# Performance work log

Measured on AMD Instinct MI355X. Metric: run time of the kernel, lower is better.

Reference implementation:

```python
import jax, jax.numpy as jnp
import numpy as np

R = 65  # num_relations


def rgcn_conv(x, edge_index, edge_type, W, root, bias):
    """PyG RGCNConv with per-relation mean aggregation.
    Aggregate-then-transform (linearity lets us swap the order):
      mean_r[n] = mean over edges e with type r, dst(e)=n of x[src(e)]
      out = sum_r mean_r @ W_r + x @ root + bias
    """
    N = x.shape[0]
    src, dst = edge_index[0], edge_index[1]
    seg = edge_type * N + dst  # composite (relation, dst) segment id
    sums = jax.ops.segment_sum(x[src], seg, num_segments=R * N)
    sums = sums.reshape(R, N, -1)  # [R, N, F]
    cnt = jax.ops.segment_sum(jnp.ones(src.shape, x.dtype), seg, num_segments=R * N)
    cnt = cnt.reshape(R, N, 1)
    mean = sums / jnp.maximum(cnt, 1.0)
    return jnp.einsum('rni,rio->no', mean, W) + x @ root + bias


def setup_inputs() -> dict:
    key = jax.random.key(0)
    ks = jax.random.split(key, 20)
    N, E, F_in, H, M = 8000, 192000, 64, 256, 64
    B = 128
    inp = {
        'x': jax.random.normal(ks[0], (N, F_in), jnp.float32),
        'edge_index': jax.random.randint(ks[1], (2, E), 0, N),
        'edge_type': jax.random.randint(ks[2], (E,), 0, R),
        'batch': jnp.sort(jax.random.randint(ks[3], (N,), 0, B)),
    }
    def glorot(k, shape):
        fan = shape[-2] + shape[-1]
        return jax.random.normal(k, shape, jnp.float32) * jnp.sqrt(2.0 / fan)
    inp['W1'] = glorot(ks[4], (R, F_in, H)); inp['root1'] = glorot(ks[5], (F_in, H)); inp['b1'] = jnp.zeros((H,), jnp.float32)
    inp['W2'] = glorot(ks[6], (R, H, H));   inp['root2'] = glorot(ks[7], (H, H));   inp['b2'] = jnp.zeros((H,), jnp.float32)
    inp['W3'] = glorot(ks[8], (R, H, H));   inp['root3'] = glorot(ks[9], (H, H));   inp['b3'] = jnp.zeros((H,), jnp.float32)
    inp['ws_w'] = glorot(ks[10], (H, 1));    inp['ws_b'] = jnp.zeros((1,), jnp.float32)
    inp['m_w1'] = glorot(ks[11], (H, M)); inp['m_b1'] = jnp.zeros((M,), jnp.float32)
    inp['m_w2'] = glorot(ks[12], (M, M)); inp['m_b2'] = jnp.zeros((M,), jnp.float32)
    inp['m_w3'] = glorot(ks[13], (M, 1)); inp['m_b3'] = jnp.zeros((1,), jnp.float32)
    return inp


def reference(x, edge_index, edge_type, batch,
              W1, root1, b1, W2, root2, b2, W3, root3, b3,
              ws_w, ws_b, m_w1, m_b1, m_w2, m_b2, m_w3, m_b3):
    B = 128  # number of graphs in the batch
    h = jax.nn.relu(rgcn_conv(x, edge_index, edge_type, W1, root1, b1))
    h = jax.nn.relu(rgcn_conv(h, edge_index, edge_type, W2, root2, b2))
    h = jax.nn.relu(rgcn_conv(h, edge_index, edge_type, W3, root3, b3))
    # WeightedSum pooling: sigmoid gate per node, scatter-sum per graph
    w = jax.nn.sigmoid(h @ ws_w + ws_b)            # [N, 1]
    pooled = jax.ops.segment_sum(w * h, batch, num_segments=B)  # [B, H]
    # MLP head
    m = jax.nn.relu(pooled @ m_w1 + m_b1)
    m = jax.nn.relu(m @ m_w2 + m_b2)
    return m @ m_w3 + m_b3                          # [B, 1]
```

## Files before the change

### kernel.cpp

```cpp
#include <hip/hip_runtime.h>

#define NNODES 8000
#define NEDGES 192000
#define NREL   65
#define RP     66
#define HDIM   256
#define FDIM   64
#define NGRAPH 128
#define MDIM   64
#define TILE_M 64
#define MAXT   3456
#define EPTOT  (NEDGES + NNODES)

typedef _Float16 half8 __attribute__((ext_vector_type(8)));
typedef _Float16 half4 __attribute__((ext_vector_type(4)));
typedef float    f32x4 __attribute__((ext_vector_type(4)));


__global__ void count_kernel(const int* __restrict__ ei, const int* __restrict__ et,
                             int* __restrict__ cnt_rn, int* __restrict__ type_cnt,
                             int* __restrict__ ddeg) {
    __shared__ int lbin[NREL];
    int tid = threadIdx.x;
    if (tid < NREL) lbin[tid] = 0;
    __syncthreads();
    int e = blockIdx.x * 256 + tid;
    if (e < NEDGES) {
        int t = et[e];
        int d = ei[NEDGES + e];
        atomicAdd(&lbin[t], 1);
        atomicAdd(&cnt_rn[t * NNODES + d], 1);
        atomicAdd(&ddeg[d], 1);
    }
    __syncthreads();
    if (tid < NREL && lbin[tid] > 0) atomicAdd(&type_cnt[tid], lbin[tid]);
}

__global__ void scan_tiles_kernel(const int* __restrict__ type_cnt, int* __restrict__ type_off,
                                  int* __restrict__ tile_rel, int* __restrict__ tile_start,
                                  int* __restrict__ tile_nrows) {
    __shared__ int s_off[RP + 1];
    __shared__ int s_toff[RP + 1];
    if (threadIdx.x == 0) {
        int off = 0, toff = 0;
        for (int r = 0; r < RP; r++) {
            int c = (r < NREL) ? type_cnt[r] : NNODES;
            s_off[r] = off; s_toff[r] = toff;
            off += c; toff += (c + TILE_M - 1) / TILE_M;
        }
        s_off[RP] = off; s_toff[RP] = toff;
        type_off[RP] = off;
    }
    __syncthreads();
    int r = threadIdx.x;
    if (r < RP) {
        type_off[r] = s_off[r];
        int c = s_off[r + 1] - s_off[r];
        int nt = (c + TILE_M - 1) / TILE_M;
        for (int i = 0; i < nt; i++) {
            int idx = s_toff[r] + i;
            tile_rel[idx]   = r;
            tile_start[idx] = s_off[r] + i * TILE_M;
            tile_nrows[idx] = min(TILE_M, c - i * TILE_M);
        }
    }
}

__global__ void dst_scan_kernel(const int* __restrict__ ddeg, int* __restrict__ dst_off) {
    __shared__ int part[256];
    int t = threadIdx.x;
    int base = t * 32;
    int s = 0;
    for (int i = 0; i < 32; i++) {
        int n = base + i;
        if (n < NNODES) s += ddeg[n] + 1;
    }
    part[t] = s;
    __syncthreads();
    if (t == 0) {
        int run = 0;
        for (int i = 0; i < 256; i++) { int tmp = part[i]; part[i] = run; run += tmp; }
        dst_off[NNODES] = run;
    }
    __syncthreads();
    int run = part[t];
    for (int i = 0; i < 32; i++) {
        int n = base + i;
        if (n < NNODES) { dst_off[n] = run; run += ddeg[n] + 1; }
    }
}

__global__ void scatter_kernel(const int* __restrict__ ei, const int* __restrict__ et,
                               const int* __restrict__ cnt_rn, const int* __restrict__ type_off,
                               int* __restrict__ type_cur,
                               const int* __restrict__ dst_off, int* __restrict__ dst_cur,
                               int* __restrict__ esrc, int* __restrict__ eq,
                               float* __restrict__ escale) {
    __shared__ int lbin[NREL];
    __shared__ int gbase[NREL];
    int tid = threadIdx.x;
    if (tid < NREL) lbin[tid] = 0;
    __syncthreads();
    int i = blockIdx.x * 256 + tid;
    int t = 0, lrank = 0;
    bool is_edge = (i < NEDGES);
    if (is_edge) {
        t = et[i];
        lrank = atomicAdd(&lbin[t], 1);
    }
    __syncthreads();
    if (tid < NREL && lbin[tid] > 0) gbase[tid] = atomicAdd(&type_cur[tid], lbin[tid]);
    __syncthreads();
    if (is_edge) {
        int d = ei[NEDGES + i];
        int p = type_off[t] + gbase[t] + lrank;
        int q = dst_off[d] + atomicAdd(&dst_cur[d], 1);
        esrc[p] = ei[i];
        eq[p] = q;
        escale[p] = 1.0f / (float)cnt_rn[t * NNODES + d];
    } else if (i < EPTOT) {
        int n = i - NEDGES;
        int p = NEDGES + n;
        int q = dst_off[n] + atomicAdd(&dst_cur[n], 1);
        esrc[p] = n; eq[p] = q; escale[p] = 1.0f;
    }
}

__global__ void convW_kernel(const float* __restrict__ W, const float* __restrict__ root,
                             _Float16* __restrict__ Wt, int K) {
    int r = blockIdx.x, k0 = blockIdx.y * 32, n0 = blockIdx.z * 32;
    const float* src = (r < NREL) ? (W + (size_t)r * K * HDIM) : root;
    __shared__ float tile[32][33];
    int tj = threadIdx.x & 31, ti = threadIdx.x >> 5;
    #pragma unroll
    for (int s = 0; s < 4; s++) {
        int i = ti + s * 8;
        tile[i][tj] = src[(size_t)(k0 + i) * HDIM + n0 + tj];
    }
    __syncthreads();
    #pragma unroll
    for (int s = 0; s < 4; s++) {
        int i = ti + s * 8;
        Wt[((size_t)r * HDIM + (n0 + i)) * K + k0 + tj] = (_Float16)tile[tj][i];
    }
}

__global__ void conv_x_kernel(const float* __restrict__ x, _Float16* __restrict__ x16) {
    int i = blockIdx.x * 256 + threadIdx.x;
    if (i < NNODES * FDIM) x16[i] = (_Float16)x[i];
}

template <int K>
__global__ __launch_bounds__(256)
void edge_gemm_kernel(const _Float16* __restrict__ hin, const _Float16* __restrict__ Wt,
                      const int* __restrict__ esrc, const int* __restrict__ eq,
                      const float* __restrict__ escale,
                      const int* __restrict__ tile_rel, const int* __restrict__ tile_start,
                      const int* __restrict__ tile_nrows,
                      _Float16* __restrict__ Y) {
    int nr = tile_nrows[blockIdx.x];
    if (nr == 0) return;
    int r  = tile_rel[blockIdx.x];
    int ts = tile_start[blockIdx.x];

    constexpr int LK = K + 8;
    constexpr int SO = HDIM + 8;
    constexpr int LMAX = (LK > SO) ? LK : SO;
    __shared__ _Float16 sbuf[TILE_M * LMAX];
    __shared__ int   sq[TILE_M];
    __shared__ float sscale[TILE_M];

    int tid = threadIdx.x;
    constexpr int CPR = K / 8;
    for (int idx = tid; idx < TILE_M * CPR; idx += 256) {
        int row = idx / CPR, c = idx % CPR;
        uint4 v = make_uint4(0, 0, 0, 0);
        if (row < nr) {
            int src = esrc[ts + row];
            v = *(const uint4*)(hin + (size_t)src * K + c * 8);
        }
        *(uint4*)&sbuf[row * LK + c * 8] = v;
    }
    if (tid < TILE_M) {
        if (tid < nr) { sq[tid] = eq[ts + tid]; sscale[tid] = escale[ts + tid]; }
        else          { sq[tid] = 0;            sscale[tid] = 0.f; }
    }
    __syncthreads();

    int lane = tid & 63, w = tid >> 6;
    int lm = lane & 15, quad = lane >> 4;
    f32x4 acc[4][4] = {};
    const _Float16* Bbase = Wt + ((size_t)r * HDIM + w * 64 + lm) * K + quad * 8;
    const _Float16* Abase = sbuf + lm * LK + quad * 8;

    for (int kk = 0; kk < K; kk += 32) {
        half8 a[4], b[4];
        #pragma unroll
        for (int mt = 0; mt < 4; mt++)
            a[mt] = *(const half8*)(Abase + mt * 16 * LK + kk);
        #pragma unroll
        for (int nt = 0; nt < 4; nt++)
            b[nt] = *(const half8*)(Bbase + nt * 16 * K + kk);
        #pragma unroll
        for (int mt = 0; mt < 4; mt++)
            #pragma unroll
            for (int nt = 0; nt < 4; nt++)
                acc[mt][nt] = __builtin_amdgcn_mfma_f32_16x16x32_f16(a[mt], b[nt], acc[mt][nt], 0, 0, 0);
    }

    __syncthreads();

    #pragma unroll
    for (int mt = 0; mt < 4; mt++) {
        #pragma unroll
        for (int rr = 0; rr < 4; rr++) {
            int row = mt * 16 + quad * 4 + rr;
            float s = sscale[row];
            #pragma unroll
            for (int nt = 0; nt < 4; nt++) {
                int col = w * 64 + nt * 16 + lm;
                sbuf[row * SO + col] = (_Float16)(acc[mt][nt][rr] * s);
            }
        }
    }
    __syncthreads();

    for (int idx = tid; idx < TILE_M * 32; idx += 256) {
        int row = idx >> 5, seg = idx & 31;
        if (row < nr) {
            uint4 v = *(const uint4*)&sbuf[row * SO + seg * 8];
            *(uint4*)(Y + (size_t)sq[row] * HDIM + seg * 8) = v;
        }
    }
}

__global__ __launch_bounds__(256)
void reduce_kernel(const _Float16* __restrict__ Y, const int* __restrict__ dst_off,
                   const float* __restrict__ bias, _Float16* __restrict__ hout) {
    int n = blockIdx.x;
    int start = dst_off[n], end = dst_off[n + 1];
    int t = threadIdx.x;
    int c = t & 31;
    int r = t >> 5;
    float acc[8] = {0, 0, 0, 0, 0, 0, 0, 0};
    for (int j = start + r; j < end; j += 8) {
        half8 v = *(const half8*)(Y + (size_t)j * HDIM + c * 8);
        #pragma unroll
        for (int k = 0; k < 8; k++) acc[k] += (float)v[k];
    }
    __shared__ float red[8][32][8];
    #pragma unroll
    for (int k = 0; k < 8; k++) red[r][c][k] = acc[k];
    __syncthreads();
    if (t < 32) {
        float a[8];
        #pragma unroll
        for (int k = 0; k < 8; k++) a[k] = red[0][t][k];
        for (int rr = 1; rr < 8; rr++)
            #pragma unroll
            for (int k = 0; k < 8; k++) a[k] += red[rr][t][k];
        half8 o;
        #pragma unroll
        for (int k = 0; k < 8; k++) {
            float v = a[k] + bias[t * 8 + k];
            o[k] = (_Float16)(v > 0.f ? v : 0.f);
        }
        *(half8*)(hout + (size_t)n * HDIM + t * 8) = o;
    }
}


__global__ void gate_kernel(const _Float16* __restrict__ h, const float* __restrict__ ws_w,
                            const float* __restrict__ ws_b, float* __restrict__ gate) {
    int node = blockIdx.x * 4 + (threadIdx.x >> 6);
    int lane = threadIdx.x & 63;
    half4 v = *(const half4*)(h + (size_t)node * HDIM + lane * 4);
    float s = 0.f;
    #pragma unroll
    for (int k = 0; k < 4; k++) s += (float)v[k] * ws_w[lane * 4 + k];
    for (int o = 32; o > 0; o >>= 1) s += __shfl_down(s, o, 64);
    if (lane == 0) gate[node] = 1.f / (1.f + __expf(-(s + ws_b[0])));
}

__global__ void pool_kernel(const _Float16* __restrict__ h, const float* __restrict__ gate,
                            const int* __restrict__ batch, float* __restrict__ pooled) {
    int g = blockIdx.x, t = threadIdx.x;
    int a = 0, b = NNODES;
    while (a < b) { int m = (a + b) >> 1; if (batch[m] < g) a = m + 1; else b = m; }
    int lo = a;
    b = NNODES;
    while (a < b) { int m = (a + b) >> 1; if (batch[m] < g + 1) a = m + 1; else b = m; }
    int hi = a;
    float acc = 0.f;
    for (int n = lo; n < hi; n++)
        acc += gate[n] * (float)h[(size_t)n * HDIM + t];
    pooled[(size_t)g * HDIM + t] = acc;
}

__global__ void head_kernel(const float* __restrict__ pooled,
                            const float* __restrict__ w1, const float* __restrict__ b1,
                            const float* __restrict__ w2, const float* __restrict__ b2,
                            const float* __restrict__ w3, const float* __restrict__ b3,
                            float* __restrict__ out) {
    int b = blockIdx.x, tid = threadIdx.x;
    __shared__ float sp[HDIM];
    __shared__ float m1[MDIM];
    __shared__ float m2[MDIM];
    for (int i = tid; i < HDIM; i += 64) sp[i] = pooled[(size_t)b * HDIM + i];
    __syncthreads();
    float a = b1[tid];
    for (int i = 0; i < HDIM; i++) a += sp[i] * w1[i * MDIM + tid];
    m1[tid] = a > 0.f ? a : 0.f;
    __syncthreads();
    float c = b2[tid];
    for (int i = 0; i < MDIM; i++) c += m1[i] * w2[i * MDIM + tid];
    m2[tid] = c > 0.f ? c : 0.f;
    __syncthreads();
    float p = m2[tid] * w3[tid];
    for (int o = 32; o > 0; o >>= 1) p += __shfl_down(p, o, 64);
    if (tid == 0) out[b] = p + b3[0];
}


extern "C" void kernel_launch(void* const* d_in, const int* in_sizes, int n_in,
                              void* d_out, int out_size, void* d_ws, size_t ws_size,
                              hipStream_t stream) {
    const float* x     = (const float*)d_in[0];
    const int*   ei    = (const int*)d_in[1];
    const int*   et    = (const int*)d_in[2];
    const int*   batch = (const int*)d_in[3];
    const float* W1    = (const float*)d_in[4];
    const float* root1 = (const float*)d_in[5];
    const float* b1    = (const float*)d_in[6];
    const float* W2    = (const float*)d_in[7];
    const float* root2 = (const float*)d_in[8];
    const float* b2    = (const float*)d_in[9];
    const float* W3    = (const float*)d_in[10];
    const float* root3 = (const float*)d_in[11];
    const float* b3    = (const float*)d_in[12];
    const float* ws_w  = (const float*)d_in[13];
    const float* ws_b  = (const float*)d_in[14];
    const float* m_w1  = (const float*)d_in[15];
    const float* m_b1  = (const float*)d_in[16];
    const float* m_w2  = (const float*)d_in[17];
    const float* m_b2  = (const float*)d_in[18];
    const float* m_w3  = (const float*)d_in[19];
    const float* m_b3  = (const float*)d_in[20];
    float* out = (float*)d_out;

    char* ws = (char*)d_ws;
    size_t o = 0;
    auto take = [&](size_t bytes) { size_t r = o; o = (o + bytes + 255) & ~(size_t)255; return r; };

    size_t o_cnt_rn = take((size_t)NREL * NNODES * 4);
    size_t o_tcnt   = take(RP * 4);
    size_t o_tcur   = take(RP * 4);
    size_t o_toff   = take((RP + 1) * 4);
    size_t o_ddeg   = take((size_t)NNODES * 4);
    size_t o_dcur   = take((size_t)NNODES * 4);
    size_t o_doff   = take((size_t)(NNODES + 1) * 4);
    size_t o_esrc   = take((size_t)EPTOT * 4);
    size_t o_eq     = take((size_t)EPTOT * 4);
    size_t o_escale = take((size_t)EPTOT * 4);
    size_t o_trel   = take(MAXT * 4);
    size_t o_tstart = take(MAXT * 4);
    size_t o_tnrows = take(MAXT * 4);
    size_t o_wt1    = take((size_t)RP * HDIM * FDIM * 2);
    size_t o_wt2    = take((size_t)RP * HDIM * HDIM * 2);
    size_t o_wt3    = take((size_t)RP * HDIM * HDIM * 2);
    size_t o_x16    = take((size_t)NNODES * FDIM * 2);
    size_t o_h16    = take((size_t)NNODES * HDIM * 2);
    size_t o_gate   = take((size_t)NNODES * 4);
    size_t o_pool   = take((size_t)NGRAPH * HDIM * 4);
    size_t o_y16    = take((size_t)EPTOT * HDIM * 2);

    int*      cnt_rn   = (int*)(ws + o_cnt_rn);
    int*      type_cnt = (int*)(ws + o_tcnt);
    int*      type_cur = (int*)(ws + o_tcur);
    int*      type_off = (int*)(ws + o_toff);
    int*      ddeg     = (int*)(ws + o_ddeg);
    int*      dst_cur  = (int*)(ws + o_dcur);
    int*      dst_off  = (int*)(ws + o_doff);
    int*      esrc     = (int*)(ws + o_esrc);
    int*      eq       = (int*)(ws + o_eq);
    float*    escale   = (float*)(ws + o_escale);
    int*      trel     = (int*)(ws + o_trel);
    int*      tstart   = (int*)(ws + o_tstart);
    int*      tnrows   = (int*)(ws + o_tnrows);
    _Float16* Wt1      = (_Float16*)(ws + o_wt1);
    _Float16* Wt2      = (_Float16*)(ws + o_wt2);
    _Float16* Wt3      = (_Float16*)(ws + o_wt3);
    _Float16* x16      = (_Float16*)(ws + o_x16);
    _Float16* h16      = (_Float16*)(ws + o_h16);
    float*    gate     = (float*)(ws + o_gate);
    float*    pooled   = (float*)(ws + o_pool);
    _Float16* Y16      = (_Float16*)(ws + o_y16);

    hipMemsetAsync(ws + o_cnt_rn, 0, o_toff - o_cnt_rn, stream);
    hipMemsetAsync(ws + o_ddeg, 0, o_doff - o_ddeg, stream);
    hipMemsetAsync(ws + o_tnrows, 0, MAXT * 4, stream);

    count_kernel<<<(NEDGES + 255) / 256, 256, 0, stream>>>(ei, et, cnt_rn, type_cnt, ddeg);
    scan_tiles_kernel<<<1, 128, 0, stream>>>(type_cnt, type_off, trel, tstart, tnrows);
    dst_scan_kernel<<<1, 256, 0, stream>>>(ddeg, dst_off);
    scatter_kernel<<<(EPTOT + 255) / 256, 256, 0, stream>>>(ei, et, cnt_rn, type_off, type_cur,
                                                            dst_off, dst_cur, esrc, eq, escale);

    convW_kernel<<<dim3(RP, FDIM / 32, HDIM / 32), 256, 0, stream>>>(W1, root1, Wt1, FDIM);
    convW_kernel<<<dim3(RP, HDIM / 32, HDIM / 32), 256, 0, stream>>>(W2, root2, Wt2, HDIM);
    convW_kernel<<<dim3(RP, HDIM / 32, HDIM / 32), 256, 0, stream>>>(W3, root3, Wt3, HDIM);
    conv_x_kernel<<<(NNODES * FDIM + 255) / 256, 256, 0, stream>>>(x, x16);

    edge_gemm_kernel<FDIM><<<MAXT, 256, 0, stream>>>(x16, Wt1, esrc, eq, escale,
                                                     trel, tstart, tnrows, Y16);
    reduce_kernel<<<NNODES, 256, 0, stream>>>(Y16, dst_off, b1, h16);

    edge_gemm_kernel<HDIM><<<MAXT, 256, 0, stream>>>(h16, Wt2, esrc, eq, escale,
                                                     trel, tstart, tnrows, Y16);
    reduce_kernel<<<NNODES, 256, 0, stream>>>(Y16, dst_off, b2, h16);

    edge_gemm_kernel<HDIM><<<MAXT, 256, 0, stream>>>(h16, Wt3, esrc, eq, escale,
                                                     trel, tstart, tnrows, Y16);
    reduce_kernel<<<NNODES, 256, 0, stream>>>(Y16, dst_off, b3, h16);

    gate_kernel<<<NNODES / 4, 256, 0, stream>>>(h16, ws_w, ws_b, gate);
    pool_kernel<<<NGRAPH, 256, 0, stream>>>(h16, gate, batch, pooled);
    head_kernel<<<NGRAPH, 64, 0, stream>>>(pooled, m_w1, m_b1, m_w2, m_b2, m_w3, m_b3, out);

    (void)in_sizes; (void)n_in; (void)out_size; (void)ws_size;
}
```

Baseline: 491.2 us.

## Bucket relation tiles by XCD and software-pipeline MFMA operand loads

Tiles are grouped into 8 buckets keyed by relation mod 8. Block IDs are then remapped so that consecutive blocks, which are dispatched round-robin across the 8 XCDs, each stay within one bucket. The intent is that all tiles of a relation run on the same XCD, so its weight slice stays in that XCD's L2. The GEMM k-loop also prefetches the next A/B fragments while the current MFMAs run, hiding load latency at some register cost. The grid grows to 4608 blocks, and more of them exit early as empty.

Result: slower. 558.1 us (+13.6%).

```diff
diff --git a/kernel.cpp b/kernel.cpp
--- a/kernel.cpp
+++ b/kernel.cpp
@@ -9,8 +9,11 @@
 #define NGRAPH 128
 #define MDIM   64
 #define TILE_M 64
-#define MAXT   3456
 #define EPTOT  (NEDGES + NNODES)
+
+#define NBKT   8
+#define BKTCAP 576
+#define GRID_G (NBKT * BKTCAP)
 
 typedef _Float16 half8 __attribute__((ext_vector_type(8)));
 typedef _Float16 half4 __attribute__((ext_vector_type(4)));
@@ -40,15 +43,20 @@
                                   int* __restrict__ tile_rel, int* __restrict__ tile_start,
                                   int* __restrict__ tile_nrows) {
     __shared__ int s_off[RP + 1];
-    __shared__ int s_toff[RP + 1];
+    __shared__ int s_bkt[RP];
     if (threadIdx.x == 0) {
-        int off = 0, toff = 0;
+        int off = 0;
+        int bcnt[NBKT];
+        for (int b = 0; b < NBKT; b++) bcnt[b] = 0;
         for (int r = 0; r < RP; r++) {
             int c = (r < NREL) ? type_cnt[r] : NNODES;
-            s_off[r] = off; s_toff[r] = toff;
-            off += c; toff += (c + TILE_M - 1) / TILE_M;
-        }
-        s_off[RP] = off; s_toff[RP] = toff;
+            s_off[r] = off; off += c;
+            int nt = (c + TILE_M - 1) / TILE_M;
+            int b = r & 7;
+            s_bkt[r] = bcnt[b];
+            bcnt[b] += nt;
+        }
+        s_off[RP] = off;
         type_off[RP] = off;
     }
     __syncthreads();
@@ -57,8 +65,9 @@
         type_off[r] = s_off[r];
         int c = s_off[r + 1] - s_off[r];
         int nt = (c + TILE_M - 1) / TILE_M;
+        int base = (r & 7) * BKTCAP + s_bkt[r];
         for (int i = 0; i < nt; i++) {
-            int idx = s_toff[r] + i;
+            int idx = base + i;
             tile_rel[idx]   = r;
             tile_start[idx] = s_off[r] + i * TILE_M;
             tile_nrows[idx] = min(TILE_M, c - i * TILE_M);
@@ -158,10 +167,11 @@
                       const int* __restrict__ tile_rel, const int* __restrict__ tile_start,
                       const int* __restrict__ tile_nrows,
                       _Float16* __restrict__ Y) {
-    int nr = tile_nrows[blockIdx.x];
+    int slot = (blockIdx.x & 7) * BKTCAP + (blockIdx.x >> 3);
+    int nr = tile_nrows[slot];
     if (nr == 0) return;
-    int r  = tile_rel[blockIdx.x];
-    int ts = tile_start[blockIdx.x];
+    int r  = tile_rel[slot];
+    int ts = tile_start[slot];
 
     constexpr int LK = K + 8;
     constexpr int SO = HDIM + 8;
@@ -193,19 +203,34 @@
     const _Float16* Bbase = Wt + ((size_t)r * HDIM + w * 64 + lm) * K + quad * 8;
     const _Float16* Abase = sbuf + lm * LK + quad * 8;
 
+    half8 bc[4], ac[4];
+    #pragma unroll
+    for (int nt = 0; nt < 4; nt++) bc[nt] = *(const half8*)(Bbase + nt * 16 * K);
+    #pragma unroll
+    for (int mt = 0; mt < 4; mt++) ac[mt] = *(const half8*)(Abase + mt * 16 * LK);
+
+    #pragma unroll
     for (int kk = 0; kk < K; kk += 32) {
-        half8 a[4], b[4];
+        half8 bn[4], an[4];
+        if (kk + 32 < K) {
+            #pragma unroll
+            for (int nt = 0; nt < 4; nt++)
+                bn[nt] = *(const half8*)(Bbase + nt * 16 * K + kk + 32);
+            #pragma unroll
+            for (int mt = 0; mt < 4; mt++)
+                an[mt] = *(const half8*)(Abase + mt * 16 * LK + kk + 32);
+        }
         #pragma unroll
         for (int mt = 0; mt < 4; mt++)
-            a[mt] = *(const half8*)(Abase + mt * 16 * LK + kk);
-        #pragma unroll
-        for (int nt = 0; nt < 4; nt++)
-            b[nt] = *(const half8*)(Bbase + nt * 16 * K + kk);
-        #pragma unroll
-        for (int mt = 0; mt < 4; mt++)
             #pragma unroll
             for (int nt = 0; nt < 4; nt++)
-                acc[mt][nt] = __builtin_amdgcn_mfma_f32_16x16x32_f16(a[mt], b[nt], acc[mt][nt], 0, 0, 0);
+                acc[mt][nt] = __builtin_amdgcn_mfma_f32_16x16x32_f16(ac[mt], bc[nt], acc[mt][nt], 0, 0, 0);
+        if (kk + 32 < K) {
+            #pragma unroll
+            for (int nt = 0; nt < 4; nt++) bc[nt] = bn[nt];
+            #pragma unroll
+            for (int mt = 0; mt < 4; mt++) ac[mt] = an[mt];
+        }
     }
 
     __syncthreads();
@@ -362,9 +387,9 @@
     size_t o_esrc   = take((size_t)EPTOT * 4);
     size_t o_eq     = take((size_t)EPTOT * 4);
     size_t o_escale = take((size_t)EPTOT * 4);
-    size_t o_trel   = take(MAXT * 4);
-    size_t o_tstart = take(MAXT * 4);
-    size_t o_tnrows = take(MAXT * 4);
+    size_t o_trel   = take(GRID_G * 4);
+    size_t o_tstart = take(GRID_G * 4);
+    size_t o_tnrows = take(GRID_G * 4);
     size_t o_wt1    = take((size_t)RP * HDIM * FDIM * 2);
     size_t o_wt2    = take((size_t)RP * HDIM * HDIM * 2);
     size_t o_wt3    = take((size_t)RP * HDIM * HDIM * 2);
@@ -398,7 +423,7 @@
 
     hipMemsetAsync(ws + o_cnt_rn, 0, o_toff - o_cnt_rn, stream);
     hipMemsetAsync(ws + o_ddeg, 0, o_doff - o_ddeg, stream);
-    hipMemsetAsync(ws + o_tnrows, 0, MAXT * 4, stream);
+    hipMemsetAsync(ws + o_tnrows, 0, GRID_G * 4, stream);
 
     count_kernel<<<(NEDGES + 255) / 256, 256, 0, stream>>>(ei, et, cnt_rn, type_cnt, ddeg);
     scan_tiles_kernel<<<1, 128, 0, stream>>>(type_cnt, type_off, trel, tstart, tnrows);
@@ -411,16 +436,16 @@
     convW_kernel<<<dim3(RP, HDIM / 32, HDIM / 32), 256, 0, stream>>>(W3, root3, Wt3, HDIM);
     conv_x_kernel<<<(NNODES * FDIM + 255) / 256, 256, 0, stream>>>(x, x16);
 
-    edge_gemm_kernel<FDIM><<<MAXT, 256, 0, stream>>>(x16, Wt1, esrc, eq, escale,
-                                                     trel, tstart, tnrows, Y16);
+    edge_gemm_kernel<FDIM><<<GRID_G, 256, 0, stream>>>(x16, Wt1, esrc, eq, escale,
+                                                       trel, tstart, tnrows, Y16);
     reduce_kernel<<<NNODES, 256, 0, stream>>>(Y16, dst_off, b1, h16);
 
-    edge_gemm_kernel<HDIM><<<MAXT, 256, 0, stream>>>(h16, Wt2, esrc, eq, escale,
-                                                     trel, tstart, tnrows, Y16);
+    edge_gemm_kernel<HDIM><<<GRID_G, 256, 0, stream>>>(h16, Wt2, esrc, eq, escale,
+                                                       trel, tstart, tnrows, Y16);
     reduce_kernel<<<NNODES, 256, 0, stream>>>(Y16, dst_off, b2, h16);
 
-    edge_gemm_kernel<HDIM><<<MAXT, 256, 0, stream>>>(h16, Wt3, esrc, eq, escale,
-                                                     trel, tstart, tnrows, Y16);
+    edge_gemm_kernel<HDIM><<<GRID_G, 256, 0, stream>>>(h16, Wt3, esrc, eq, escale,
+                                                       trel, tstart, tnrows, Y16);
     reduce_kernel<<<NNODES, 256, 0, stream>>>(Y16, dst_off, b3, h16);
 
     gate_kernel<<<NNODES / 4, 256, 0, stream>>>(h16, ws_w, ws_b, gate);
```

## Enlarge edge GEMM tiles to 128 rows with 8 waves and register prefetch

Applied to the files above, without the earlier changes.

The edge GEMM tile doubles from 64 to 128 edge rows and runs on 512 threads, so 8 waves split the tile into two row halves and four column quarters. Each relation's weight slice read from global memory now feeds twice as many rows, which cuts weight traffic and launches about half as many blocks. The K loop also loads the next A and B fragments into registers before issuing the current MFMAs, to hide load latency. The cost is roughly twice the LDS per block, fewer resident blocks, more padded rows on each relation's last tile, and a larger MAXT bound that has to stay consistent with the tile scan.

After: 545.1 us. 1.11x slower.

```diff
diff --git a/kernel.cpp b/kernel.cpp
--- a/kernel.cpp
+++ b/kernel.cpp
@@ -8,9 +8,10 @@
 #define FDIM   64
 #define NGRAPH 128
 #define MDIM   64
-#define TILE_M 64
-#define MAXT   3456
+#define TILE_M 128
+#define MAXT   1792
 #define EPTOT  (NEDGES + NNODES)
+
 
 typedef _Float16 half8 __attribute__((ext_vector_type(8)));
 typedef _Float16 half4 __attribute__((ext_vector_type(4)));
@@ -151,7 +152,7 @@
 }
 
 template <int K>
-__global__ __launch_bounds__(256)
+__global__ __launch_bounds__(512)
 void edge_gemm_kernel(const _Float16* __restrict__ hin, const _Float16* __restrict__ Wt,
                       const int* __restrict__ esrc, const int* __restrict__ eq,
                       const float* __restrict__ escale,
@@ -172,7 +173,7 @@
 
     int tid = threadIdx.x;
     constexpr int CPR = K / 8;
-    for (int idx = tid; idx < TILE_M * CPR; idx += 256) {
+    for (int idx = tid; idx < TILE_M * CPR; idx += 512) {
         int row = idx / CPR, c = idx % CPR;
         uint4 v = make_uint4(0, 0, 0, 0);
         if (row < nr) {
@@ -188,24 +189,40 @@
     __syncthreads();
 
     int lane = tid & 63, w = tid >> 6;
+    int rh = w >> 2, cq = w & 3;
     int lm = lane & 15, quad = lane >> 4;
     f32x4 acc[4][4] = {};
-    const _Float16* Bbase = Wt + ((size_t)r * HDIM + w * 64 + lm) * K + quad * 8;
-    const _Float16* Abase = sbuf + lm * LK + quad * 8;
-
+    const _Float16* Bbase = Wt + ((size_t)r * HDIM + cq * 64 + lm) * K + quad * 8;
+    const _Float16* Abase = sbuf + (rh * 64 + lm) * LK + quad * 8;
+
+    half8 bc[4], ac[4];
+    #pragma unroll
+    for (int nt = 0; nt < 4; nt++) bc[nt] = *(const half8*)(Bbase + nt * 16 * K);
+    #pragma unroll
+    for (int mt = 0; mt < 4; mt++) ac[mt] = *(const half8*)(Abase + mt * 16 * LK);
+
+    #pragma unroll
     for (int kk = 0; kk < K; kk += 32) {
-        half8 a[4], b[4];
+        half8 bn[4], an[4];
+        if (kk + 32 < K) {
+            #pragma unroll
+            for (int nt = 0; nt < 4; nt++)
+                bn[nt] = *(const half8*)(Bbase + nt * 16 * K + kk + 32);
+            #pragma unroll
+            for (int mt = 0; mt < 4; mt++)
+                an[mt] = *(const half8*)(Abase + mt * 16 * LK + kk + 32);
+        }
         #pragma unroll
         for (int mt = 0; mt < 4; mt++)
-            a[mt] = *(const half8*)(Abase + mt * 16 * LK + kk);
-        #pragma unroll
-        for (int nt = 0; nt < 4; nt++)
-            b[nt] = *(const half8*)(Bbase + nt * 16 * K + kk);
-        #pragma unroll
-        for (int mt = 0; mt < 4; mt++)
             #pragma unroll
             for (int nt = 0; nt < 4; nt++)
-                acc[mt][nt] = __builtin_amdgcn_mfma_f32_16x16x32_f16(a[mt], b[nt], acc[mt][nt], 0, 0, 0);
+                acc[mt][nt] = __builtin_amdgcn_mfma_f32_16x16x32_f16(ac[mt], bc[nt], acc[mt][nt], 0, 0, 0);
+        if (kk + 32 < K) {
+            #pragma unroll
+            for (int nt = 0; nt < 4; nt++) bc[nt] = bn[nt];
+            #pragma unroll
+            for (int mt = 0; mt < 4; mt++) ac[mt] = an[mt];
+        }
     }
 
     __syncthreads();
@@ -214,18 +231,18 @@
     for (int mt = 0; mt < 4; mt++) {
         #pragma unroll
         for (int rr = 0; rr < 4; rr++) {
-            int row = mt * 16 + quad * 4 + rr;
+            int row = rh * 64 + mt * 16 + quad * 4 + rr;
             float s = sscale[row];
             #pragma unroll
             for (int nt = 0; nt < 4; nt++) {
-                int col = w * 64 + nt * 16 + lm;
+                int col = cq * 64 + nt * 16 + lm;
                 sbuf[row * SO + col] = (_Float16)(acc[mt][nt][rr] * s);
             }
         }
     }
     __syncthreads();
 
-    for (int idx = tid; idx < TILE_M * 32; idx += 256) {
+    for (int idx = tid; idx < TILE_M * 32; idx += 512) {
         int row = idx >> 5, seg = idx & 31;
         if (row < nr) {
             uint4 v = *(const uint4*)&sbuf[row * SO + seg * 8];
@@ -411,15 +428,15 @@
     convW_kernel<<<dim3(RP, HDIM / 32, HDIM / 32), 256, 0, stream>>>(W3, root3, Wt3, HDIM);
     conv_x_kernel<<<(NNODES * FDIM + 255) / 256, 256, 0, stream>>>(x, x16);
 
-    edge_gemm_kernel<FDIM><<<MAXT, 256, 0, stream>>>(x16, Wt1, esrc, eq, escale,
+    edge_gemm_kernel<FDIM><<<MAXT, 512, 0, stream>>>(x16, Wt1, esrc, eq, escale,
                                                      trel, tstart, tnrows, Y16);
     reduce_kernel<<<NNODES, 256, 0, stream>>>(Y16, dst_off, b1, h16);
 
-    edge_gemm_kernel<HDIM><<<MAXT, 256, 0, stream>>>(h16, Wt2, esrc, eq, escale,
+    edge_gemm_kernel<HDIM><<<MAXT, 512, 0, stream>>>(h16, Wt2, esrc, eq, escale,
                                                      trel, tstart, tnrows, Y16);
     reduce_kernel<<<NNODES, 256, 0, stream>>>(Y16, dst_off, b2, h16);
 
-    edge_gemm_kernel<HDIM><<<MAXT, 256, 0, stream>>>(h16, Wt3, esrc, eq, escale,
+    edge_gemm_kernel<HDIM><<<MAXT, 512, 0, stream>>>(h16, Wt3, esrc, eq, escale,
                                                      trel, tstart, tnrows, Y16);
     reduce_kernel<<<NNODES, 256, 0, stream>>>(Y16, dst_off, b3, h16);
 
```
